# Performance work log

Hardware: AMD Instinct MI355X
Metric: run time of the kernel (lower is better)

Reference implementation:

```python
import jax, jax.numpy as jnp
import numpy as np

INNER_STEPS = 50
INNER_LR = 0.1
Y_MEAN = 0.0


def _mlp(params, inp):
    # eqx.nn.MLP(in=3, out=1, width=64, depth=3): relu hidden, identity final
    W1, b1, W2, b2, W3, b3, W4, b4 = params
    h = jax.nn.relu(W1 @ inp + b1)
    h = jax.nn.relu(W2 @ h + b2)
    h = jax.nn.relu(W3 @ h + b3)
    return jnp.squeeze(W4 @ h + b4)


def setup_inputs() -> dict:
    key = jax.random.key(0)
    ks = jax.random.split(key, 10)
    B, CD, W = 8192, 1, 64
    d_in = 2 + CD
    x = jax.random.normal(ks[0], (B, 1), dtype=jnp.float32)
    c = jax.random.normal(ks[1], (B, CD), dtype=jnp.float32)
    def lin(k, fan_out, fan_in):
        lim = 1.0 / np.sqrt(fan_in)
        kw, kb = jax.random.split(k)
        Wm = jax.random.uniform(kw, (fan_out, fan_in), minval=-lim, maxval=lim, dtype=jnp.float32)
        bm = jax.random.uniform(kb, (fan_out,), minval=-lim, maxval=lim, dtype=jnp.float32)
        return Wm, bm
    W1, b1 = lin(ks[2], W, d_in)
    W2, b2 = lin(ks[3], W, W)
    W3, b3 = lin(ks[4], W, W)
    W4, b4 = lin(ks[5], 1, W)
    return {"x": x, "c": c, "W1": W1, "b1": b1, "W2": W2, "b2": b2,
            "W3": W3, "b3": b3, "W4": W4, "b4": b4}


def reference(x, c, W1, b1, W2, b2, W3, b3, W4, b4):
    params = (W1, b1, W2, b2, W3, b3, W4, b4)
    # nearest-neighbor c0 per sample (excluding self)
    dists = jnp.linalg.norm(c[:, None, :] - c[None, :, :], axis=-1)  # [B,B]
    dists = dists + jnp.eye(dists.shape[0], dtype=dists.dtype) * 1e9
    c0 = c[jnp.argmin(dists, axis=1)]  # [B,CD]

    def base_energy(xi, yi, ci):
        return _mlp(params, jnp.concatenate([xi, yi, ci], axis=0))

    def solve(xi, ci, c0i):
        y0 = jnp.array([Y_MEAN], dtype=xi.dtype)

        def step(y, _):
            def loss(yy):
                E0, dE = jax.jvp(lambda cc: base_energy(xi, yy, cc), (c0i,), (ci - c0i,))
                return E0 + dE
            gy = jax.grad(loss)(y)
            return y - INNER_LR * gy, None

        yf, _ = jax.lax.scan(step, y0, None, length=INNER_STEPS)
        return yf

    return jax.vmap(solve)(x, c, c0)  # [B,1]
```

## Files before the change

### kernel.cpp

```cpp
#include <hip/hip_runtime.h>

#define BATCH 8192
#define LOSC  2048.0f
#define LOINV (1.0f / 2048.0f)

typedef _Float16 f16x4 __attribute__((ext_vector_type(4)));
typedef __fp16   fp16x2 __attribute__((ext_vector_type(2)));
typedef float    f32x4 __attribute__((ext_vector_type(4)));

union PK2 { fp16x2 h; unsigned u; };
union U4  { f16x4 v; unsigned u[2]; };

__device__ __forceinline__ unsigned pkrtz(float a, float b) {
    PK2 p; p.h = __builtin_amdgcn_cvt_pkrtz(a, b); return p.u;
}
__device__ __forceinline__ float lo0(unsigned hp, float v) {
    PK2 p; p.u = hp; return (v - (float)p.h[0]) * LOSC;
}
__device__ __forceinline__ float lo1(unsigned hp, float v) {
    PK2 p; p.u = hp; return (v - (float)p.h[1]) * LOSC;
}

__global__ __launch_bounds__(256) void nn_kernel(const float* __restrict__ c,
                                                 float* __restrict__ c0) {
    __shared__ float cs[BATCH];
    const int t = threadIdx.x;
    {
        const float4* cg = (const float4*)c;
        float4* cl = (float4*)cs;
        for (int j = t; j < BATCH / 4; j += 256) cl[j] = cg[j];
    }
    __syncthreads();
    const int part = t & 31;
    const int i    = blockIdx.x * 8 + (t >> 5);
    const float ci = cs[i];
    const int sj0 = ((i & 3) == 0) ? (i >> 2) : -1;
    const int sj1 = ((i & 3) == 1) ? (i >> 2) : -1;
    const int sj2 = ((i & 3) == 2) ? (i >> 2) : -1;
    const int sj3 = ((i & 3) == 3) ? (i >> 2) : -1;
    const float4* cs4 = (const float4*)cs;
    float bd0 = 3e38f, bd1 = 3e38f, bd2 = 3e38f, bd3 = 3e38f;
    int   bj0 = 0,     bj1 = 0,     bj2 = 0,     bj3 = 0;
    #pragma unroll 4
    for (int tt = 0; tt < 64; ++tt) {
        const int jj = part + (tt << 5);
        const float4 v = cs4[jj];
        float d0 = fabsf(ci - v.x);
        float d1 = fabsf(ci - v.y);
        float d2 = fabsf(ci - v.z);
        float d3 = fabsf(ci - v.w);
        if (jj == sj0) d0 = 3e38f;
        if (jj == sj1) d1 = 3e38f;
        if (jj == sj2) d2 = 3e38f;
        if (jj == sj3) d3 = 3e38f;
        if (d0 < bd0) { bd0 = d0; bj0 = jj; }
        if (d1 < bd1) { bd1 = d1; bj1 = jj; }
        if (d2 < bd2) { bd2 = d2; bj2 = jj; }
        if (d3 < bd3) { bd3 = d3; bj3 = jj; }
    }
    float best = bd0; int bestj = bj0 * 4 + 0;
    { const int j1 = bj1 * 4 + 1; if (bd1 < best || (bd1 == best && j1 < bestj)) { best = bd1; bestj = j1; } }
    { const int j2 = bj2 * 4 + 2; if (bd2 < best || (bd2 == best && j2 < bestj)) { best = bd2; bestj = j2; } }
    { const int j3 = bj3 * 4 + 3; if (bd3 < best || (bd3 == best && j3 < bestj)) { best = bd3; bestj = j3; } }
    #pragma unroll
    for (int off = 1; off < 32; off <<= 1) {
        const float od = __shfl_xor(best, off);
        const int   oj = __shfl_xor(bestj, off);
        if (od < best || (od == best && oj < bestj)) { best = od; bestj = oj; }
    }
    if (part == 0) c0[i] = cs[bestj];
}

__global__ __launch_bounds__(64, 1) void solve_kernel(
    const float* __restrict__ x, const float* __restrict__ c0g,
    const float* __restrict__ W1, const float* __restrict__ b1,
    const float* __restrict__ W2, const float* __restrict__ b2,
    const float* __restrict__ W3, const float* __restrict__ b3,
    const float* __restrict__ W4, float* __restrict__ out)
{
    const int lane = threadIdx.x & 63;
    const int q  = lane >> 4;
    const int cc = lane & 15;
    const bool fwd = (cc < 8);
    const int s = cc & 7;
    const int sbase = blockIdx.x * 8;

    f16x4 W2h[4][4], W2l[4][4], W3h[4][4], W3l[4][4];
    #pragma unroll
    for (int T = 0; T < 4; ++T)
        #pragma unroll
        for (int m = 0; m < 4; ++m) {
            const int off = (T * 16 + cc) * 64 + m * 16 + q * 4;
            const float4 w2 = *(const float4*)(W2 + off);
            const float4 w3 = *(const float4*)(W3 + off);
            U4 h, l;
            h.u[0] = pkrtz(w2.x, w2.y); h.u[1] = pkrtz(w2.z, w2.w);
            l.u[0] = pkrtz(lo0(h.u[0], w2.x), lo1(h.u[0], w2.y));
            l.u[1] = pkrtz(lo0(h.u[1], w2.z), lo1(h.u[1], w2.w));
            W2h[T][m] = h.v; W2l[T][m] = l.v;
            h.u[0] = pkrtz(w3.x, w3.y); h.u[1] = pkrtz(w3.z, w3.w);
            l.u[0] = pkrtz(lo0(h.u[0], w3.x), lo1(h.u[0], w3.y));
            l.u[1] = pkrtz(lo0(h.u[1], w3.z), lo1(h.u[1], w3.w));
            W3h[T][m] = h.v; W3l[T][m] = l.v;
        }

    float b2m[16], b3m[16], w4r[16];
    #pragma unroll
    for (int T = 0; T < 4; ++T)
        #pragma unroll
        for (int r = 0; r < 4; ++r) {
            const int row = T * 16 + q * 4 + r;
            b2m[T * 4 + r] = fwd ? b2[row] : 0.f;
            b3m[T * 4 + r] = fwd ? b3[row] : 0.f;
            w4r[T * 4 + r] = W4[row];
        }

    float A1v[16], w11v[16];
    {
        const float xs  = x[sbase + s];
        const float c0s = c0g[sbase + s];
        #pragma unroll
        for (int m = 0; m < 4; ++m)
            #pragma unroll
            for (int j = 0; j < 4; ++j) {
                const int k = m * 16 + q * 4 + j;
                w11v[m * 4 + j] = W1[k * 3 + 1];
                A1v[m * 4 + j]  = fmaf(xs, W1[k * 3 + 0],
                                       fmaf(c0s, W1[k * 3 + 2], b1[k]));
            }
    }

    float y = 0.0f;

    #pragma unroll 1
    for (int step = 0; step < 50; ++step) {
        U4 B1h[4], B1l[4];
        #pragma unroll
        for (int m = 0; m < 4; ++m) {
            float v[4];
            #pragma unroll
            for (int j = 0; j < 4; ++j) {
                const float w = w11v[m * 4 + j];
                const float z = fmaf(y, w, A1v[m * 4 + j]);
                v[j] = fwd ? fmaxf(z, 0.f) : (z > 0.f ? w : 0.f);
            }
            const unsigned h0 = pkrtz(v[0], v[1]);
            const unsigned h1 = pkrtz(v[2], v[3]);
            B1h[m].u[0] = h0; B1h[m].u[1] = h1;
            B1l[m].u[0] = pkrtz(lo0(h0, v[0]), lo1(h0, v[1]));
            B1l[m].u[1] = pkrtz(lo0(h1, v[2]), lo1(h1, v[3]));
        }
        f32x4 ZH[4], ZL[4];
        #pragma unroll
        for (int T = 0; T < 4; ++T) {
            f32x4 aH;
            aH[0] = b2m[T * 4 + 0]; aH[1] = b2m[T * 4 + 1];
            aH[2] = b2m[T * 4 + 2]; aH[3] = b2m[T * 4 + 3];
            f32x4 aL = {0.f, 0.f, 0.f, 0.f};
            #pragma unroll
            for (int m = 0; m < 4; ++m) {
                aH = __builtin_amdgcn_mfma_f32_16x16x16f16(W2h[T][m], B1h[m].v, aH, 0, 0, 0);
                aL = __builtin_amdgcn_mfma_f32_16x16x16f16(W2h[T][m], B1l[m].v, aL, 0, 0, 0);
                aL = __builtin_amdgcn_mfma_f32_16x16x16f16(W2l[T][m], B1h[m].v, aL, 0, 0, 0);
            }
            ZH[T] = aH; ZL[T] = aL;
        }
        U4 B2h[4], B2l[4];
        #pragma unroll
        for (int T = 0; T < 4; ++T) {
            float v[4];
            #pragma unroll
            for (int r = 0; r < 4; ++r) {
                const float z = fmaf(ZL[T][r], LOINV, ZH[T][r]);
                const float recv = __shfl_xor(z, 8);
                v[r] = fwd ? fmaxf(z, 0.f) : (recv > 0.f ? z : 0.f);
            }
            const unsigned h0 = pkrtz(v[0], v[1]);
            const unsigned h1 = pkrtz(v[2], v[3]);
            B2h[T].u[0] = h0; B2h[T].u[1] = h1;
            B2l[T].u[0] = pkrtz(lo0(h0, v[0]), lo1(h0, v[1]));
            B2l[T].u[1] = pkrtz(lo0(h1, v[2]), lo1(h1, v[3]));
        }
        #pragma unroll
        for (int T = 0; T < 4; ++T) {
            f32x4 aH;
            aH[0] = b3m[T * 4 + 0]; aH[1] = b3m[T * 4 + 1];
            aH[2] = b3m[T * 4 + 2]; aH[3] = b3m[T * 4 + 3];
            f32x4 aL = {0.f, 0.f, 0.f, 0.f};
            #pragma unroll
            for (int m = 0; m < 4; ++m) {
                aH = __builtin_amdgcn_mfma_f32_16x16x16f16(W3h[T][m], B2h[m].v, aH, 0, 0, 0);
                aL = __builtin_amdgcn_mfma_f32_16x16x16f16(W3h[T][m], B2l[m].v, aL, 0, 0, 0);
                aL = __builtin_amdgcn_mfma_f32_16x16x16f16(W3l[T][m], B2h[m].v, aL, 0, 0, 0);
            }
            ZH[T] = aH; ZL[T] = aL;
        }
        float g = 0.f;
        #pragma unroll
        for (int T = 0; T < 4; ++T)
            #pragma unroll
            for (int r = 0; r < 4; ++r) {
                const float z = fmaf(ZL[T][r], LOINV, ZH[T][r]);
                const float recv  = __shfl_xor(z, 8);
                const float maskv = fwd ? z : recv;
                const float valv  = fwd ? recv : z;
                g = fmaf(w4r[T * 4 + r], (maskv > 0.f) ? valv : 0.f, g);
            }
        g += __shfl_xor(g, 16);
        g += __shfl_xor(g, 32);
        y -= 0.1f * g;
    }
    if (lane < 8) out[sbase + lane] = y;
}

extern "C" void kernel_launch(void* const* d_in, const int* in_sizes, int n_in,
                              void* d_out, int out_size, void* d_ws, size_t ws_size,
                              hipStream_t stream) {
    const float* x  = (const float*)d_in[0];
    const float* c  = (const float*)d_in[1];
    const float* W1 = (const float*)d_in[2];
    const float* b1 = (const float*)d_in[3];
    const float* W2 = (const float*)d_in[4];
    const float* b2 = (const float*)d_in[5];
    const float* W3 = (const float*)d_in[6];
    const float* b3 = (const float*)d_in[7];
    const float* W4 = (const float*)d_in[8];
    float* c0  = (float*)d_ws;
    float* out = (float*)d_out;

    nn_kernel<<<BATCH / 8, 256, 0, stream>>>(c, c0);
    solve_kernel<<<BATCH / 8, 64, 0, stream>>>(x, c0, W1, b1, W2, b2, W3, b3, W4, out);
}
```

Before: 168.6 us.

## Fuse nearest-neighbor search into solve kernel and batch cross-lane shuffles

Drops the separate nn_kernel. Each 64-lane solve block now loads all of c into shared memory and computes the nearest neighbor for its own 8 samples, using 8 lanes per sample, before the solve loop. This removes a kernel launch and the c0 round trip through global memory. In exchange each single-wave block loads 32KB of LDS and does a longer serial scan, which may limit occupancy and add latency. The solve loop also gathers all 16 shuffle-xor exchanges per layer ahead of the activation math so they can be issued together.

```diff
diff --git a/kernel.cpp b/kernel.cpp
--- a/kernel.cpp
+++ b/kernel.cpp
@@ -21,69 +21,74 @@
     PK2 p; p.u = hp; return (v - (float)p.h[1]) * LOSC;
 }
 
-__global__ __launch_bounds__(256) void nn_kernel(const float* __restrict__ c,
-                                                 float* __restrict__ c0) {
-    __shared__ float cs[BATCH];
-    const int t = threadIdx.x;
-    {
-        const float4* cg = (const float4*)c;
-        float4* cl = (float4*)cs;
-        for (int j = t; j < BATCH / 4; j += 256) cl[j] = cg[j];
-    }
-    __syncthreads();
-    const int part = t & 31;
-    const int i    = blockIdx.x * 8 + (t >> 5);
-    const float ci = cs[i];
-    const int sj0 = ((i & 3) == 0) ? (i >> 2) : -1;
-    const int sj1 = ((i & 3) == 1) ? (i >> 2) : -1;
-    const int sj2 = ((i & 3) == 2) ? (i >> 2) : -1;
-    const int sj3 = ((i & 3) == 3) ? (i >> 2) : -1;
-    const float4* cs4 = (const float4*)cs;
-    float bd0 = 3e38f, bd1 = 3e38f, bd2 = 3e38f, bd3 = 3e38f;
-    int   bj0 = 0,     bj1 = 0,     bj2 = 0,     bj3 = 0;
-    #pragma unroll 4
-    for (int tt = 0; tt < 64; ++tt) {
-        const int jj = part + (tt << 5);
-        const float4 v = cs4[jj];
-        float d0 = fabsf(ci - v.x);
-        float d1 = fabsf(ci - v.y);
-        float d2 = fabsf(ci - v.z);
-        float d3 = fabsf(ci - v.w);
-        if (jj == sj0) d0 = 3e38f;
-        if (jj == sj1) d1 = 3e38f;
-        if (jj == sj2) d2 = 3e38f;
-        if (jj == sj3) d3 = 3e38f;
-        if (d0 < bd0) { bd0 = d0; bj0 = jj; }
-        if (d1 < bd1) { bd1 = d1; bj1 = jj; }
-        if (d2 < bd2) { bd2 = d2; bj2 = jj; }
-        if (d3 < bd3) { bd3 = d3; bj3 = jj; }
-    }
-    float best = bd0; int bestj = bj0 * 4 + 0;
-    { const int j1 = bj1 * 4 + 1; if (bd1 < best || (bd1 == best && j1 < bestj)) { best = bd1; bestj = j1; } }
-    { const int j2 = bj2 * 4 + 2; if (bd2 < best || (bd2 == best && j2 < bestj)) { best = bd2; bestj = j2; } }
-    { const int j3 = bj3 * 4 + 3; if (bd3 < best || (bd3 == best && j3 < bestj)) { best = bd3; bestj = j3; } }
-    #pragma unroll
-    for (int off = 1; off < 32; off <<= 1) {
-        const float od = __shfl_xor(best, off);
-        const int   oj = __shfl_xor(bestj, off);
-        if (od < best || (od == best && oj < bestj)) { best = od; bestj = oj; }
-    }
-    if (part == 0) c0[i] = cs[bestj];
-}
-
 __global__ __launch_bounds__(64, 1) void solve_kernel(
-    const float* __restrict__ x, const float* __restrict__ c0g,
+    const float* __restrict__ x, const float* __restrict__ c,
     const float* __restrict__ W1, const float* __restrict__ b1,
     const float* __restrict__ W2, const float* __restrict__ b2,
     const float* __restrict__ W3, const float* __restrict__ b3,
     const float* __restrict__ W4, float* __restrict__ out)
 {
+    __shared__ float cs[BATCH];
+
     const int lane = threadIdx.x & 63;
     const int q  = lane >> 4;
     const int cc = lane & 15;
     const bool fwd = (cc < 8);
     const int s = cc & 7;
     const int sbase = blockIdx.x * 8;
+
+    {
+        const float4* cg = (const float4*)c;
+        float4* cl = (float4*)cs;
+        #pragma unroll 4
+        for (int w = lane; w < BATCH / 4; w += 64) cl[w] = cg[w];
+    }
+    __syncthreads();
+
+    float c0s;
+    {
+        const int il = lane >> 3;
+        const int p  = lane & 7;
+        const int ni = sbase + il;
+        const float ci = cs[ni];
+        const int iw = ni >> 2;
+        const int sj0 = (((iw & 7) == p) && ((ni & 3) == 0)) ? iw : -1;
+        const int sj1 = (((iw & 7) == p) && ((ni & 3) == 1)) ? iw : -1;
+        const int sj2 = (((iw & 7) == p) && ((ni & 3) == 2)) ? iw : -1;
+        const int sj3 = (((iw & 7) == p) && ((ni & 3) == 3)) ? iw : -1;
+        const float4* cs4 = (const float4*)cs;
+        float bd0 = 3e38f, bd1 = 3e38f, bd2 = 3e38f, bd3 = 3e38f;
+        int   bj0 = 0,     bj1 = 0,     bj2 = 0,     bj3 = 0;
+        #pragma unroll 4
+        for (int t = 0; t < 256; ++t) {
+            const int jj = p + (t << 3);
+            const float4 v = cs4[jj];
+            float d0 = fabsf(ci - v.x);
+            float d1 = fabsf(ci - v.y);
+            float d2 = fabsf(ci - v.z);
+            float d3 = fabsf(ci - v.w);
+            if (jj == sj0) d0 = 3e38f;
+            if (jj == sj1) d1 = 3e38f;
+            if (jj == sj2) d2 = 3e38f;
+            if (jj == sj3) d3 = 3e38f;
+            if (d0 < bd0) { bd0 = d0; bj0 = jj; }
+            if (d1 < bd1) { bd1 = d1; bj1 = jj; }
+            if (d2 < bd2) { bd2 = d2; bj2 = jj; }
+            if (d3 < bd3) { bd3 = d3; bj3 = jj; }
+        }
+        float best = bd0; int bestj = bj0 * 4 + 0;
+        { const int j1 = bj1 * 4 + 1; if (bd1 < best || (bd1 == best && j1 < bestj)) { best = bd1; bestj = j1; } }
+        { const int j2 = bj2 * 4 + 2; if (bd2 < best || (bd2 == best && j2 < bestj)) { best = bd2; bestj = j2; } }
+        { const int j3 = bj3 * 4 + 3; if (bd3 < best || (bd3 == best && j3 < bestj)) { best = bd3; bestj = j3; } }
+        #pragma unroll
+        for (int off = 1; off < 8; off <<= 1) {
+            const float od = __shfl_xor(best, off);
+            const int   oj = __shfl_xor(bestj, off);
+            if (od < best || (od == best && oj < bestj)) { best = od; bestj = oj; }
+        }
+        const float c0grp = cs[bestj];
+        c0s = __shfl(c0grp, s * 8);
+    }
 
     f16x4 W2h[4][4], W2l[4][4], W3h[4][4], W3l[4][4];
     #pragma unroll
@@ -117,8 +122,7 @@
 
     float A1v[16], w11v[16];
     {
-        const float xs  = x[sbase + s];
-        const float c0s = c0g[sbase + s];
+        const float xs = x[sbase + s];
         #pragma unroll
         for (int m = 0; m < 4; ++m)
             #pragma unroll
@@ -165,15 +169,21 @@
             }
             ZH[T] = aH; ZL[T] = aL;
         }
+        float z2[16], rc2[16];
+        #pragma unroll
+        for (int k = 0; k < 16; ++k)
+            z2[k] = fmaf(ZL[k >> 2][k & 3], LOINV, ZH[k >> 2][k & 3]);
+        #pragma unroll
+        for (int k = 0; k < 16; ++k)
+            rc2[k] = __shfl_xor(z2[k], 8);
         U4 B2h[4], B2l[4];
         #pragma unroll
         for (int T = 0; T < 4; ++T) {
             float v[4];
             #pragma unroll
             for (int r = 0; r < 4; ++r) {
-                const float z = fmaf(ZL[T][r], LOINV, ZH[T][r]);
-                const float recv = __shfl_xor(z, 8);
-                v[r] = fwd ? fmaxf(z, 0.f) : (recv > 0.f ? z : 0.f);
+                const float z = z2[T * 4 + r];
+                v[r] = fwd ? fmaxf(z, 0.f) : (rc2[T * 4 + r] > 0.f ? z : 0.f);
             }
             const unsigned h0 = pkrtz(v[0], v[1]);
             const unsigned h1 = pkrtz(v[2], v[3]);
@@ -195,17 +205,20 @@
             }
             ZH[T] = aH; ZL[T] = aL;
         }
+        float z3[16], rc3[16];
+        #pragma unroll
+        for (int k = 0; k < 16; ++k)
+            z3[k] = fmaf(ZL[k >> 2][k & 3], LOINV, ZH[k >> 2][k & 3]);
+        #pragma unroll
+        for (int k = 0; k < 16; ++k)
+            rc3[k] = __shfl_xor(z3[k], 8);
         float g = 0.f;
         #pragma unroll
-        for (int T = 0; T < 4; ++T)
-            #pragma unroll
-            for (int r = 0; r < 4; ++r) {
-                const float z = fmaf(ZL[T][r], LOINV, ZH[T][r]);
-                const float recv  = __shfl_xor(z, 8);
-                const float maskv = fwd ? z : recv;
-                const float valv  = fwd ? recv : z;
-                g = fmaf(w4r[T * 4 + r], (maskv > 0.f) ? valv : 0.f, g);
-            }
+        for (int k = 0; k < 16; ++k) {
+            const float maskv = fwd ? z3[k] : rc3[k];
+            const float valv  = fwd ? rc3[k] : z3[k];
+            g = fmaf(w4r[k], (maskv > 0.f) ? valv : 0.f, g);
+        }
         g += __shfl_xor(g, 16);
         g += __shfl_xor(g, 32);
         y -= 0.1f * g;
@@ -225,9 +238,7 @@
     const float* W3 = (const float*)d_in[6];
     const float* b3 = (const float*)d_in[7];
     const float* W4 = (const float*)d_in[8];
-    float* c0  = (float*)d_ws;
     float* out = (float*)d_out;
 
-    nn_kernel<<<BATCH / 8, 256, 0, stream>>>(c, c0);
-    solve_kernel<<<BATCH / 8, 64, 0, stream>>>(x, c0, W1, b1, W2, b2, W3, b3, W4, out);
-}
+    solve_kernel<<<BATCH / 8, 64, 0, stream>>>(x, c, W1, b1, W2, b2, W3, b3, W4, out);
+}
```

Result: slower. 179.4 us (+6.4%).
